# Performance work log

Measured on AMD Instinct MI355X. Metric: run time of the kernel, lower is better.

## Reference

```python
import jax, jax.numpy as jnp
import numpy as np
import math

N, E, C, NB, NEL, NG = 8192, 131072, 64, 8, 4, 16
R_MAX, AVG_NEI, P_CUT, NL, SH = 5.0, 16.0, 6, 2, 16


def _sph(u):
    # real spherical harmonics l=0..3, component normalization (sum_m Y_lm^2 = 2l+1 on unit sphere)
    x, y, z = u[:, 0], u[:, 1], u[:, 2]
    s3, s15, s5 = math.sqrt(3.0), math.sqrt(15.0), math.sqrt(5.0)
    s105, s7 = math.sqrt(105.0), math.sqrt(7.0)
    c35, c21 = math.sqrt(35.0 / 8.0), math.sqrt(21.0 / 8.0)
    Y = [jnp.ones_like(x),
         s3 * x, s3 * y, s3 * z,
         s15 * x * y, s15 * y * z, 0.5 * s5 * (3 * z * z - 1), s15 * x * z, 0.5 * s15 * (x * x - y * y),
         c35 * y * (3 * x * x - y * y), s105 * x * y * z, c21 * y * (5 * z * z - 1),
         0.5 * s7 * (5 * z ** 3 - 3 * z), c21 * x * (5 * z * z - 1),
         0.5 * s105 * z * (x * x - y * y), c35 * x * (x * x - 3 * y * y)]
    return jnp.stack(Y, axis=-1)  # [E,16]


def _bessel(r):
    k = jnp.arange(1, NB + 1, dtype=r.dtype)
    return math.sqrt(2.0 / R_MAX) * jnp.sin(k * jnp.pi * r[:, None] / R_MAX) / r[:, None]


def _poly_cutoff(r):
    p = float(P_CUT)
    x = r / R_MAX
    f = (1.0 - 0.5 * (p + 1) * (p + 2) * x ** p + p * (p + 2) * x ** (p + 1)
         - 0.5 * p * (p + 1) * x ** (p + 2))
    return f * (x < 1.0)


def setup_inputs() -> dict:
    key = jax.random.key(0)
    ks = jax.random.split(key, 16)
    sc = lambda fan: 1.0 / math.sqrt(fan)
    return {
        "pos": 2.0 * jax.random.normal(ks[0], (N, 3), jnp.float32),
        "atom_types": jax.random.randint(ks[1], (N,), 0, NEL),
        "edge_index": jax.random.randint(ks[2], (2, E), 0, N),
        "batch": jnp.sort(jax.random.randint(ks[3], (N,), 0, NG)),
        "W_embed": jax.random.normal(ks[4], (NEL, C), jnp.float32),
        "W_r1": sc(NB) * jax.random.normal(ks[5], (NL, NB, 64), jnp.float32),
        "W_r2": sc(64) * jax.random.normal(ks[6], (NL, 64, 64), jnp.float32),
        "W_r3": sc(64) * jax.random.normal(ks[7], (NL, 64, C), jnp.float32),
        "W_sc": sc(C) * jax.random.normal(ks[8], (NL, NEL, C, C), jnp.float32),
        "w_prod": 0.5 * jax.random.normal(ks[9], (NL, NEL, 4), jnp.float32),
        "w_ro0": sc(C) * jax.random.normal(ks[10], (C,), jnp.float32),
        "W_ro1a": sc(C) * jax.random.normal(ks[11], (C, 16), jnp.float32),
        "w_ro1b": sc(16) * jax.random.normal(ks[12], (16,), jnp.float32),
    }


def reference(pos, atom_types, edge_index, batch, W_embed, W_r1, W_r2, W_r3,
              W_sc, w_prod, w_ro0, W_ro1a, w_ro1b):
    src, dst = edge_index[0], edge_index[1]
    vec = pos[dst] - pos[src]                      # [E,3]
    r = jnp.sqrt(jnp.sum(vec * vec, -1) + 1e-12)   # [E]
    Y = _sph(vec / r[:, None])                     # [E,SH]
    edge_feats = _bessel(r) * _poly_cutoff(r)[:, None]  # [E,NB]
    h = W_embed[atom_types]                        # one-hot @ W == lookup, [N,C]
    energies = [jnp.zeros((NG,), pos.dtype)]       # pair_repulsion disabled
    for i in range(NL):
        Rw = jax.nn.silu(edge_feats @ W_r1[i])
        Rw = jax.nn.silu(Rw @ W_r2[i])
        Rw = Rw @ W_r3[i]                          # radial MLP weights [E,C]
        # gather-TP-scatter: message [E,C,SH] -> node A [N,C,SH]
        m = (Rw * h[src])[:, :, None] * Y[:, None, :]
        A = jax.ops.segment_sum(m.reshape(E, C * SH), dst,
                                num_segments=N).reshape(N, C, SH) / AVG_NEI
        sc_feat = jnp.einsum('nc,ncd->nd', h, W_sc[i][atom_types])  # element-dep skip
        inv = jnp.stack([A[:, :, 0],
                         jnp.sum(A[:, :, 1:4] ** 2, -1),
                         jnp.sum(A[:, :, 4:9] ** 2, -1),
                         jnp.sum(A[:, :, 9:16] ** 2, -1)], axis=-1)  # [N,C,4]
        h = jnp.einsum('ncj,nj->nc', inv, w_prod[i][atom_types]) + sc_feat
        if i < NL - 1:
            e_node = h @ w_ro0                     # linear readout
        else:
            e_node = jax.nn.silu(h @ W_ro1a) @ w_ro1b  # gated MLP readout
        energies.append(jax.ops.segment_sum(e_node, batch, num_segments=NG))
    contributions = jnp.stack(energies, -1)        # [NG, NL+1]
    return jnp.sum(contributions, -1)              # total energy per graph
```

## Files before the change

### kernel.cpp

```cpp
#include <hip/hip_runtime.h>
#include <hip/hip_bf16.h>
#include <math.h>

#define N_NODES 8192
#define N_EDGES 131072
#define NGRP 16
#define NLAY 2
#define NELM 4
constexpr float INV_AVG = 1.0f / 16.0f;
constexpr float PI_F = 3.14159265358979323846f;

#define CV_POS   0
#define CV_EMB   24576
#define CV_SC    42240
#define CV_PROD  75008
#define CV_RO0   75040
#define CV_RO1A  75104
#define CV_RO1B  76128
#define CVT_N    76144

#define SWZ_PER_L 10240
#define SWZ_N     20480

#define B_CVT  230
#define B_SWZ  80
#define B_HIST 512
#define CVT_WORK 58736

typedef __hip_bfloat16 bf16;
typedef __attribute__((ext_vector_type(8))) short bf16x8;
typedef __attribute__((ext_vector_type(4))) float f32x4;

__device__ __forceinline__ float silu_f(float x){ return x / (1.0f + __expf(-x)); }
__device__ __forceinline__ float bfbits2f(unsigned short u){
  return __uint_as_float(((unsigned)u) << 16);
}
__device__ __forceinline__ void unpack2(unsigned u, float& lo, float& hi){
  lo = __uint_as_float(u << 16);
  hi = __uint_as_float(u & 0xffff0000u);
}
__device__ __forceinline__ short f2bs(float v){
  union { bf16 b; short s; } u; u.b = __float2bfloat16(v); return u.s;
}
__device__ __forceinline__ float ldf(const void* p, int i, int flag){
  if (flag) return bfbits2f(((const unsigned short*)p)[i]);
  return ((const float*)p)[i];
}
__device__ __forceinline__ int detect_fl(const void* pos){
  int lane = threadIdx.x & 63;
  const unsigned short* u = (const unsigned short*)pos;
  float va = bfbits2f(u[2*lane]), vb = bfbits2f(u[2*lane+1]);
  bool bad = !(fabsf(va) <= 1000.0f) || !(fabsf(vb) <= 1000.0f);
  return (__ballot(bad) == 0ull) ? 1 : 0;
}
__device__ __forceinline__ void WSYNC(){ __builtin_amdgcn_wave_barrier(); }

__device__ __forceinline__ void gl_lds4(const void* g, void* l){
  __builtin_amdgcn_global_load_lds(
      (const __attribute__((address_space(1))) unsigned*)g,
      (__attribute__((address_space(3))) unsigned*)l, 4, 0, 0);
}

__global__ void k_setup1(const void* __restrict__ pos, const void* __restrict__ Wemb,
                         const void* __restrict__ Wsc, const void* __restrict__ wprod,
                         const void* __restrict__ wro0, const void* __restrict__ Wro1a,
                         const void* __restrict__ wro1b, const void* __restrict__ Wr1,
                         const void* __restrict__ Wr2, const void* __restrict__ Wr3,
                         const int* __restrict__ dstp, float* __restrict__ cv,
                         short* __restrict__ swz, int* __restrict__ deg){
  int b = blockIdx.x, tix = threadIdx.x;
  if (b >= B_CVT + B_SWZ){
    int e = (b - B_CVT - B_SWZ)*256 + tix;
    atomicAdd(&deg[dstp[e]], 1);
    return;
  }
  int fl = detect_fl(pos);
  if (b < B_CVT){
    int i = b*256 + tix;
    if (i < 24576){ cv[CV_POS + i] = ldf(pos, i, fl); return; }
    if (i < 24832){ int j=i-24576; cv[CV_EMB + j] = ldf(Wemb, j, fl); return; }
    if (i < 57600){ int j=i-24832; cv[CV_SC  + j] = ldf(Wsc,  j, fl); return; }
    if (i < 57632){ int j=i-57600; cv[CV_PROD+ j] = ldf(wprod,j, fl); return; }
    if (i < 57696){ int j=i-57632; cv[CV_RO0 + j] = ldf(wro0, j, fl); return; }
    if (i < 58720){ int j=i-57696; cv[CV_RO1A+ j] = ldf(Wro1a,j, fl); return; }
    if (i < CVT_WORK){ int j=i-58720; cv[CV_RO1B+ j] = ldf(wro1b,j, fl); return; }
    return;
  }
  int i = (b - B_CVT)*256 + tix;
  int l = i / SWZ_PER_L, w = i % SWZ_PER_L;
  float v;
  if (w < 2048){
    int t = w >> 9, q = (w >> 7) & 3, n = (w >> 3) & 15, j = w & 7;
    int k = q*8 + j;
    v = (k < 8) ? ldf(Wr1, l*512 + k*64 + t*16 + n, fl) : 0.0f;
  } else if (w < 6144){
    int w2 = w - 2048;
    int nt = w2 >> 10, kt = (w2 >> 9) & 1, q = (w2 >> 7) & 3, n = (w2 >> 3) & 15, j = w2 & 7;
    int k = kt*32 + q*8 + j;
    v = ldf(Wr2, l*4096 + k*64 + nt*16 + n, fl);
  } else {
    int w3 = w - 6144;
    int nt = w3 >> 10, kt = (w3 >> 9) & 1, q = (w3 >> 7) & 3, n = (w3 >> 3) & 15, j = w3 & 7;
    int k = kt*32 + q*8 + j;
    v = ldf(Wr3, l*4096 + k*64 + nt*16 + n, fl);
  }
  swz[i] = f2bs(v);
}

__global__ void k_scan(const int* __restrict__ deg, int* __restrict__ row_start,
                       int* __restrict__ cursor, float* __restrict__ ene){
  __shared__ int lds[1024];
  int t = threadIdx.x;
  if (t < NGRP) ene[t] = 0.0f;
  int v[8]; int tot = 0;
#pragma unroll
  for (int k = 0; k < 8; k++){ v[k] = deg[t*8+k]; tot += v[k]; }
  lds[t] = tot; __syncthreads();
  for (int off = 1; off < 1024; off <<= 1){
    int x = (t >= off) ? lds[t-off] : 0;
    __syncthreads();
    lds[t] += x;
    __syncthreads();
  }
  int base = lds[t] - tot;
#pragma unroll
  for (int k = 0; k < 8; k++){ row_start[t*8+k] = base; cursor[t*8+k] = base; base += v[k]; }
  if (t == 1023) row_start[N_NODES] = base;
}

__global__ void k_fillgeom(const int* __restrict__ ei, int* __restrict__ cursor,
                           const float* __restrict__ posf, const int* __restrict__ types,
                           int* __restrict__ sslot, unsigned char* __restrict__ tsl,
                           unsigned short* __restrict__ Yb, float* __restrict__ rbuf){
  int e = blockIdx.x*256 + threadIdx.x;
  int s = ei[e], d = ei[N_EDGES + e];
  int slot = atomicAdd(&cursor[d], 1);
  sslot[slot] = s;
  tsl[slot] = (unsigned char)types[s];
  float vx = posf[d*3+0] - posf[s*3+0];
  float vy = posf[d*3+1] - posf[s*3+1];
  float vz = posf[d*3+2] - posf[s*3+2];
  float r = sqrtf(vx*vx + vy*vy + vz*vz + 1e-12f);
  float ir = 1.0f / r;
  float x = vx*ir, y = vy*ir, z = vz*ir;
  const float s3 = 1.7320508075688772f, s15 = 3.872983346207417f, s5 = 2.23606797749979f;
  const float s105 = 10.246950765959598f, s7 = 2.6457513110645907f;
  const float c35 = 2.091650066335189f, c21 = 1.6201851746019651f;
  float x2 = x*x, y2 = y*y, z2 = z*z;
  float ys[16] = {
    1.0f, s3*x, s3*y, s3*z,
    s15*x*y, s15*y*z, 0.5f*s5*(3.0f*z2-1.0f), s15*x*z,
    0.5f*s15*(x2-y2), c35*y*(3.0f*x2-y2), s105*x*y*z, c21*y*(5.0f*z2-1.0f),
    0.5f*s7*(5.0f*z2*z-3.0f*z), c21*x*(5.0f*z2-1.0f), 0.5f*s105*z*(x2-y2),
    c35*x*(x2-3.0f*y2) };
  union { bf16 b[16]; uint4 u[2]; } pk;
#pragma unroll
  for (int k = 0; k < 16; k++) pk.b[k] = __float2bfloat16(ys[k]);
  uint4* yp = (uint4*)(Yb + (size_t)slot*16);
  yp[0] = pk.u[0];
  yp[1] = pk.u[1];
  rbuf[slot] = r;
}

#define ROWS 72
template<int LAYER_KIND>
__global__ void __launch_bounds__(256) k_gu(const short* __restrict__ sw,
        const float* __restrict__ rbuf, const unsigned char* __restrict__ tsl,
        const int* __restrict__ sslot, const float* __restrict__ h_old,
        float* __restrict__ h_new, const unsigned short* __restrict__ Yb,
        const int* __restrict__ row_start, const int* __restrict__ types,
        const float* __restrict__ Wsc, const float* __restrict__ wprod,
        const float* __restrict__ wemb, const float* __restrict__ wro0,
        const float* __restrict__ Wro1a, const float* __restrict__ wro1b,
        const int* __restrict__ batch, float* __restrict__ ene){
  __shared__ __align__(16) short A_[4][16*ROWS];
  __shared__ __align__(16) float hS[LAYER_KIND ? 4 : 1][16][64];
  __shared__ __align__(16) unsigned short yS[4][16][16];
  __shared__ float ebins[NGRP];
  __shared__ float hn_l[LAYER_KIND ? 4 : 1][64];
  int tix = threadIdx.x;
  if (tix < NGRP) ebins[tix] = 0.0f;
  __syncthreads();
  int wv = tix >> 6, lane = tix & 63;
  int q = lane >> 4, nn = lane & 15;
  int n = blockIdx.x * 4 + wv;
  int beg = row_start[n], end = row_start[n + 1];
  short* A = A_[wv];

  const bf16x8* S1 = (const bf16x8*)(sw);
  const bf16x8* S2 = (const bf16x8*)(sw + 2048);
  const bf16x8* S3 = (const bf16x8*)(sw + 6144);

  float e0=0.f, e1=0.f, e2=0.f, e3=0.f;
  if (LAYER_KIND == 0){
    e0 = wemb[lane]; e1 = wemb[64+lane]; e2 = wemb[128+lane]; e3 = wemb[192+lane];
  }

  float acc[16];
#pragma unroll
  for (int s = 0; s < 16; s++) acc[s] = 0.0f;

  for (int cb = beg; cb < end; cb += 16){
    int cnt = min(16, end - cb);
    WSYNC();
    const char* ysrc = (const char*)Yb + (size_t)cb*32 + lane*4;
    gl_lds4(ysrc,       &yS[wv][0][0]);
    gl_lds4(ysrc + 256, &yS[wv][8][0]);
    int tv = 0;
    if (LAYER_KIND == 0){
      tv = (int)tsl[min(cb + nn, N_EDGES - 1)];
    } else {
      int sv = sslot[min(cb + nn, N_EDGES - 1)];
      for (int i = 0; i < cnt; i++){
        int src = __builtin_amdgcn_readlane(sv, i);
        gl_lds4(h_old + (size_t)src*64 + lane, &hS[wv][i][0]);
      }
    }
    {
      float r = rbuf[min(cb + nn, N_EDGES - 1)];
      float xc = r * 0.2f;
      float f = 0.0f;
      if (xc < 1.0f){
        float x3 = xc*xc*xc, x6 = x3*x3, x7 = x6*xc, x8 = x7*xc;
        f = 1.0f - 28.0f*x6 + 48.0f*x7 - 21.0f*x8;
      }
      float bs = 0.6324555320336759f * f / r;
      float t0 = PI_F * r * 0.2f;
      bf16x8 af1 = {0,0,0,0,0,0,0,0};
      if (q == 0){
#pragma unroll
        for (int j = 0; j < 8; j++) af1[j] = f2bs(bs * __sinf((float)(j+1) * t0));
      }
      f32x4 macc[4];
#pragma unroll
      for (int t = 0; t < 4; t++){
        bf16x8 b = S1[t*64 + q*16 + nn];
        f32x4 z = {0.f,0.f,0.f,0.f};
        macc[t] = __builtin_amdgcn_mfma_f32_16x16x32_bf16(af1, b, z, 0, 0, 0);
      }
#pragma unroll
      for (int t = 0; t < 4; t++)
#pragma unroll
        for (int rg = 0; rg < 4; rg++)
          A[(q*4+rg)*ROWS + t*16 + nn] = f2bs(silu_f(macc[t][rg]));
      WSYNC();
      bf16x8 a0 = *(const bf16x8*)&A[nn*ROWS + 0*32 + q*8];
      bf16x8 a1 = *(const bf16x8*)&A[nn*ROWS + 1*32 + q*8];
      WSYNC();
#pragma unroll
      for (int t = 0; t < 4; t++){
        f32x4 z = {0.f,0.f,0.f,0.f};
        bf16x8 b0 = S2[t*128 + 0*64 + q*16 + nn];
        bf16x8 b1 = S2[t*128 + 1*64 + q*16 + nn];
        z = __builtin_amdgcn_mfma_f32_16x16x32_bf16(a0, b0, z, 0, 0, 0);
        z = __builtin_amdgcn_mfma_f32_16x16x32_bf16(a1, b1, z, 0, 0, 0);
        macc[t] = z;
      }
#pragma unroll
      for (int t = 0; t < 4; t++)
#pragma unroll
        for (int rg = 0; rg < 4; rg++)
          A[(q*4+rg)*ROWS + t*16 + nn] = f2bs(silu_f(macc[t][rg]));
      WSYNC();
      a0 = *(const bf16x8*)&A[nn*ROWS + 0*32 + q*8];
      a1 = *(const bf16x8*)&A[nn*ROWS + 1*32 + q*8];
      WSYNC();
#pragma unroll
      for (int t = 0; t < 4; t++){
        f32x4 z = {0.f,0.f,0.f,0.f};
        bf16x8 b0 = S3[t*128 + 0*64 + q*16 + nn];
        bf16x8 b1 = S3[t*128 + 1*64 + q*16 + nn];
        z = __builtin_amdgcn_mfma_f32_16x16x32_bf16(a0, b0, z, 0, 0, 0);
        z = __builtin_amdgcn_mfma_f32_16x16x32_bf16(a1, b1, z, 0, 0, 0);
        macc[t] = z;
      }
#pragma unroll
      for (int t = 0; t < 4; t++)
#pragma unroll
        for (int rg = 0; rg < 4; rg++)
          A[(q*4+rg)*ROWS + t*16 + nn] = f2bs(macc[t][rg]);
      WSYNC();
    }
    asm volatile("s_waitcnt vmcnt(0)" ::: "memory");
    __builtin_amdgcn_sched_barrier(0);
    for (int i = 0; i < cnt; i++){
      float rw = bfbits2f((unsigned short)A[i*ROWS + lane]);
      float hv;
      if (LAYER_KIND == 0){
        int ty = __builtin_amdgcn_readlane(tv, i);
        hv = (ty & 2) ? ((ty & 1) ? e3 : e2) : ((ty & 1) ? e1 : e0);
      } else {
        hv = hS[wv][i][lane];
      }
      float g = rw * hv;
      const uint4* yq = (const uint4*)&yS[wv][i][0];
      uint4 ya = yq[0], yb = yq[1];
      float lo, hi;
      unpack2(ya.x, lo, hi); acc[0]  += g*lo; acc[1]  += g*hi;
      unpack2(ya.y, lo, hi); acc[2]  += g*lo; acc[3]  += g*hi;
      unpack2(ya.z, lo, hi); acc[4]  += g*lo; acc[5]  += g*hi;
      unpack2(ya.w, lo, hi); acc[6]  += g*lo; acc[7]  += g*hi;
      unpack2(yb.x, lo, hi); acc[8]  += g*lo; acc[9]  += g*hi;
      unpack2(yb.y, lo, hi); acc[10] += g*lo; acc[11] += g*hi;
      unpack2(yb.z, lo, hi); acc[12] += g*lo; acc[13] += g*hi;
      unpack2(yb.w, lo, hi); acc[14] += g*lo; acc[15] += g*hi;
    }
  }
#pragma unroll
  for (int s = 0; s < 16; s++) acc[s] *= INV_AVG;

  int ty = __builtin_amdgcn_readfirstlane(types[n]);
  const float* Ws = Wsc + (size_t)ty*4096;
  const float* hrow = (LAYER_KIND == 0) ? (wemb + ty*64) : (h_old + (size_t)n*64);
  float sc0 = 0.f, sc1 = 0.f, sc2 = 0.f, sc3 = 0.f;
#pragma unroll
  for (int c = 0; c < 64; c += 4){
    sc0 += hrow[c+0] * Ws[(c+0)*64 + lane];
    sc1 += hrow[c+1] * Ws[(c+1)*64 + lane];
    sc2 += hrow[c+2] * Ws[(c+2)*64 + lane];
    sc3 += hrow[c+3] * Ws[(c+3)*64 + lane];
  }
  float sc = (sc0 + sc1) + (sc2 + sc3);

  float inv0 = acc[0];
  float inv1 = acc[1]*acc[1] + acc[2]*acc[2] + acc[3]*acc[3];
  float inv2 = acc[4]*acc[4] + acc[5]*acc[5] + acc[6]*acc[6] + acc[7]*acc[7]
             + acc[8]*acc[8];
  float inv3 = acc[9]*acc[9] + acc[10]*acc[10] + acc[11]*acc[11] + acc[12]*acc[12]
             + acc[13]*acc[13] + acc[14]*acc[14] + acc[15]*acc[15];
  const float* wp = wprod + ty*4;
  float hn = inv0*wp[0] + inv1*wp[1] + inv2*wp[2] + inv3*wp[3] + sc;
  if (LAYER_KIND == 0)
    h_new[(size_t)n*64 + lane] = hn;

  float ev;
  if (LAYER_KIND == 0){
    float p = hn * wro0[lane];
#pragma unroll
    for (int off = 32; off >= 1; off >>= 1) p += __shfl_xor(p, off, 64);
    ev = p;
  } else {
    hn_l[wv][lane] = hn;
    int j = lane & 15;
    float pj = 0.0f;
#pragma unroll
    for (int c = 0; c < 64; c++)
      pj += hn_l[wv][c] * Wro1a[c*16 + j];
    float evj = silu_f(pj) * wro1b[j];
    evj += __shfl_xor(evj, 8, 64);
    evj += __shfl_xor(evj, 4, 64);
    evj += __shfl_xor(evj, 2, 64);
    evj += __shfl_xor(evj, 1, 64);
    ev = evj;
  }
  if (lane == 0) atomicAdd(&ebins[batch[n]], ev);
  __syncthreads();
  if (tix < NGRP){
    float v = ebins[tix];
    if (v != 0.0f) atomicAdd(&ene[tix], v);
  }
}

__global__ void k_out(const float* __restrict__ ene, const void* __restrict__ pos,
                      void* __restrict__ out){
  int fl = detect_fl(pos);
  int t = threadIdx.x;
  if (t < NGRP){
    if (fl) ((bf16*)out)[t] = __float2bfloat16(ene[t]);
    else    ((float*)out)[t] = ene[t];
  }
}

static inline size_t rup(size_t x){ return (x + 255) & ~(size_t)255; }

extern "C" void kernel_launch(void* const* d_in, const int* in_sizes, int n_in,
                              void* d_out, int out_size, void* d_ws, size_t ws_size,
                              hipStream_t stream) {
  const void* pos   = d_in[0];
  const int*  types = (const int*)d_in[1];
  const int*  ei    = (const int*)d_in[2];
  const int*  batch = (const int*)d_in[3];
  const void* Wemb  = d_in[4];
  const void* Wr1   = d_in[5];
  const void* Wr2   = d_in[6];
  const void* Wr3   = d_in[7];
  const void* Wsc   = d_in[8];
  const void* wprod = d_in[9];
  const void* wro0  = d_in[10];
  const void* Wro1a = d_in[11];
  const void* wro1b = d_in[12];

  char* w = (char*)d_ws;
  float* cv       = (float*)w; w += rup((size_t)CVT_N*4);
  short* swz      = (short*)w; w += rup((size_t)SWZ_N*2);
  float* ene      = (float*)w; w += 256;
  int*   deg      = (int*)  w; w += rup((size_t)N_NODES*4);
  int*   row_start= (int*)  w; w += rup((size_t)(N_NODES+1)*4);
  int*   cursor   = (int*)  w; w += rup((size_t)N_NODES*4);
  int*   sslot    = (int*)  w; w += rup((size_t)N_EDGES*4);
  unsigned char* tsl = (unsigned char*)w; w += rup((size_t)N_EDGES);
  float* hbuf     = (float*)w; w += rup((size_t)N_NODES*64*4);
  float* rbuf     = (float*)w; w += rup((size_t)N_EDGES*4);
  unsigned short* Yb = (unsigned short*)w; w += rup((size_t)N_EDGES*16*2);
  w += 4096;

  hipMemsetAsync(deg, 0, N_NODES*4, stream);

  const int* dstp = ei + N_EDGES;
  k_setup1<<<B_CVT + B_SWZ + B_HIST, 256, 0, stream>>>(
      pos, Wemb, Wsc, wprod, wro0, Wro1a, wro1b, Wr1, Wr2, Wr3, dstp, cv, swz, deg);
  k_scan<<<1, 1024, 0, stream>>>(deg, row_start, cursor, ene);
  k_fillgeom<<<N_EDGES/256, 256, 0, stream>>>(ei, cursor, cv + CV_POS, types,
      sslot, tsl, Yb, rbuf);

  k_gu<0><<<N_NODES/4, 256, 0, stream>>>(swz, rbuf, tsl, sslot,
      hbuf , hbuf , Yb, row_start, types,
      cv + CV_SC, cv + CV_PROD, cv + CV_EMB,
      cv + CV_RO0, cv + CV_RO1A, cv + CV_RO1B, batch, ene);
  k_gu<1><<<N_NODES/4, 256, 0, stream>>>(swz + SWZ_PER_L, rbuf, tsl, sslot,
      hbuf , hbuf , Yb, row_start, types,
      cv + CV_SC + (size_t)NELM*4096, cv + CV_PROD + NELM*4, cv + CV_EMB,
      cv + CV_RO0, cv + CV_RO1A, cv + CV_RO1B, batch, ene);

  k_out<<<1, 64, 0, stream>>>(ene, pos, d_out);
}
```

Before: 200.7 us.

## Run one wave per node block and spread energy atomics over eight bins

The gather-update kernels now launch one 64-thread block per node instead of four waves per 256-thread block. The per-block LDS energy bins and the __syncthreads barriers go away. Each node's energy is atomically added into one of eight replicated global bin sets, chosen by node index, and k_out sums the eight sets at the end. The aim is to stop fast waves waiting on slow, high-degree nodes in the same block, and to spread atomic contention. The cost is more global atomics and more, smaller blocks, which may raise scheduling overhead.

After: 191.0 us. -4.8%, faster.

```diff
diff --git a/kernel.cpp b/kernel.cpp
--- a/kernel.cpp
+++ b/kernel.cpp
@@ -108,10 +108,10 @@
 }
 
 __global__ void k_scan(const int* __restrict__ deg, int* __restrict__ row_start,
-                       int* __restrict__ cursor, float* __restrict__ ene){
+                       int* __restrict__ cursor, float* __restrict__ ene2){
   __shared__ int lds[1024];
   int t = threadIdx.x;
-  if (t < NGRP) ene[t] = 0.0f;
+  if (t < 8*NGRP) ene2[t] = 0.0f;
   int v[8]; int tot = 0;
 #pragma unroll
   for (int k = 0; k < 8; k++){ v[k] = deg[t*8+k]; tot += v[k]; }
@@ -164,7 +164,7 @@
 
 #define ROWS 72
 template<int LAYER_KIND>
-__global__ void __launch_bounds__(256) k_gu(const short* __restrict__ sw,
+__global__ void __launch_bounds__(64, 4) k_gu(const short* __restrict__ sw,
         const float* __restrict__ rbuf, const unsigned char* __restrict__ tsl,
         const int* __restrict__ sslot, const float* __restrict__ h_old,
         float* __restrict__ h_new, const unsigned short* __restrict__ Yb,
@@ -172,20 +172,16 @@
         const float* __restrict__ Wsc, const float* __restrict__ wprod,
         const float* __restrict__ wemb, const float* __restrict__ wro0,
         const float* __restrict__ Wro1a, const float* __restrict__ wro1b,
-        const int* __restrict__ batch, float* __restrict__ ene){
-  __shared__ __align__(16) short A_[4][16*ROWS];
-  __shared__ __align__(16) float hS[LAYER_KIND ? 4 : 1][16][64];
-  __shared__ __align__(16) unsigned short yS[4][16][16];
-  __shared__ float ebins[NGRP];
-  __shared__ float hn_l[LAYER_KIND ? 4 : 1][64];
-  int tix = threadIdx.x;
-  if (tix < NGRP) ebins[tix] = 0.0f;
-  __syncthreads();
-  int wv = tix >> 6, lane = tix & 63;
+        const int* __restrict__ batch, float* __restrict__ ene2){
+  __shared__ __align__(16) short A_[16*ROWS];
+  __shared__ __align__(16) float hS[LAYER_KIND ? 16 : 1][64];
+  __shared__ __align__(16) unsigned short yS[16][16];
+  __shared__ float hn_l[64];
+  int lane = threadIdx.x;
   int q = lane >> 4, nn = lane & 15;
-  int n = blockIdx.x * 4 + wv;
+  int n = blockIdx.x;
   int beg = row_start[n], end = row_start[n + 1];
-  short* A = A_[wv];
+  short* A = A_;
 
   const bf16x8* S1 = (const bf16x8*)(sw);
   const bf16x8* S2 = (const bf16x8*)(sw + 2048);
@@ -204,8 +200,8 @@
     int cnt = min(16, end - cb);
     WSYNC();
     const char* ysrc = (const char*)Yb + (size_t)cb*32 + lane*4;
-    gl_lds4(ysrc,       &yS[wv][0][0]);
-    gl_lds4(ysrc + 256, &yS[wv][8][0]);
+    gl_lds4(ysrc,       &yS[0][0]);
+    gl_lds4(ysrc + 256, &yS[8][0]);
     int tv = 0;
     if (LAYER_KIND == 0){
       tv = (int)tsl[min(cb + nn, N_EDGES - 1)];
@@ -213,7 +209,7 @@
       int sv = sslot[min(cb + nn, N_EDGES - 1)];
       for (int i = 0; i < cnt; i++){
         int src = __builtin_amdgcn_readlane(sv, i);
-        gl_lds4(h_old + (size_t)src*64 + lane, &hS[wv][i][0]);
+        gl_lds4(h_old + (size_t)src*64 + lane, &hS[i][0]);
       }
     }
     {
@@ -290,10 +286,10 @@
         int ty = __builtin_amdgcn_readlane(tv, i);
         hv = (ty & 2) ? ((ty & 1) ? e3 : e2) : ((ty & 1) ? e1 : e0);
       } else {
-        hv = hS[wv][i][lane];
+        hv = hS[i][lane];
       }
       float g = rw * hv;
-      const uint4* yq = (const uint4*)&yS[wv][i][0];
+      const uint4* yq = (const uint4*)&yS[i][0];
       uint4 ya = yq[0], yb = yq[1];
       float lo, hi;
       unpack2(ya.x, lo, hi); acc[0]  += g*lo; acc[1]  += g*hi;
@@ -340,12 +336,13 @@
     for (int off = 32; off >= 1; off >>= 1) p += __shfl_xor(p, off, 64);
     ev = p;
   } else {
-    hn_l[wv][lane] = hn;
+    hn_l[lane] = hn;
+    WSYNC();
     int j = lane & 15;
     float pj = 0.0f;
 #pragma unroll
     for (int c = 0; c < 64; c++)
-      pj += hn_l[wv][c] * Wro1a[c*16 + j];
+      pj += hn_l[c] * Wro1a[c*16 + j];
     float evj = silu_f(pj) * wro1b[j];
     evj += __shfl_xor(evj, 8, 64);
     evj += __shfl_xor(evj, 4, 64);
@@ -353,21 +350,19 @@
     evj += __shfl_xor(evj, 1, 64);
     ev = evj;
   }
-  if (lane == 0) atomicAdd(&ebins[batch[n]], ev);
-  __syncthreads();
-  if (tix < NGRP){
-    float v = ebins[tix];
-    if (v != 0.0f) atomicAdd(&ene[tix], v);
-  }
-}
-
-__global__ void k_out(const float* __restrict__ ene, const void* __restrict__ pos,
+  if (lane == 0) atomicAdd(&ene2[(n & 7)*NGRP + batch[n]], ev);
+}
+
+__global__ void k_out(const float* __restrict__ ene2, const void* __restrict__ pos,
                       void* __restrict__ out){
   int fl = detect_fl(pos);
   int t = threadIdx.x;
   if (t < NGRP){
-    if (fl) ((bf16*)out)[t] = __float2bfloat16(ene[t]);
-    else    ((float*)out)[t] = ene[t];
+    float v = 0.0f;
+#pragma unroll
+    for (int k = 0; k < 8; k++) v += ene2[k*NGRP + t];
+    if (fl) ((bf16*)out)[t] = __float2bfloat16(v);
+    else    ((float*)out)[t] = v;
   }
 }
 
@@ -393,7 +388,7 @@
   char* w = (char*)d_ws;
   float* cv       = (float*)w; w += rup((size_t)CVT_N*4);
   short* swz      = (short*)w; w += rup((size_t)SWZ_N*2);
-  float* ene      = (float*)w; w += 256;
+  float* ene2     = (float*)w; w += 512;
   int*   deg      = (int*)  w; w += rup((size_t)N_NODES*4);
   int*   row_start= (int*)  w; w += rup((size_t)(N_NODES+1)*4);
   int*   cursor   = (int*)  w; w += rup((size_t)N_NODES*4);
@@ -409,18 +404,18 @@
   const int* dstp = ei + N_EDGES;
   k_setup1<<<B_CVT + B_SWZ + B_HIST, 256, 0, stream>>>(
       pos, Wemb, Wsc, wprod, wro0, Wro1a, wro1b, Wr1, Wr2, Wr3, dstp, cv, swz, deg);
-  k_scan<<<1, 1024, 0, stream>>>(deg, row_start, cursor, ene);
+  k_scan<<<1, 1024, 0, stream>>>(deg, row_start, cursor, ene2);
   k_fillgeom<<<N_EDGES/256, 256, 0, stream>>>(ei, cursor, cv + CV_POS, types,
       sslot, tsl, Yb, rbuf);
 
-  k_gu<0><<<N_NODES/4, 256, 0, stream>>>(swz, rbuf, tsl, sslot,
+  k_gu<0><<<N_NODES, 64, 0, stream>>>(swz, rbuf, tsl, sslot,
       hbuf , hbuf , Yb, row_start, types,
       cv + CV_SC, cv + CV_PROD, cv + CV_EMB,
-      cv + CV_RO0, cv + CV_RO1A, cv + CV_RO1B, batch, ene);
-  k_gu<1><<<N_NODES/4, 256, 0, stream>>>(swz + SWZ_PER_L, rbuf, tsl, sslot,
+      cv + CV_RO0, cv + CV_RO1A, cv + CV_RO1B, batch, ene2);
+  k_gu<1><<<N_NODES, 64, 0, stream>>>(swz + SWZ_PER_L, rbuf, tsl, sslot,
       hbuf , hbuf , Yb, row_start, types,
       cv + CV_SC + (size_t)NELM*4096, cv + CV_PROD + NELM*4, cv + CV_EMB,
-      cv + CV_RO0, cv + CV_RO1A, cv + CV_RO1B, batch, ene);
-
-  k_out<<<1, 64, 0, stream>>>(ene, pos, d_out);
-}
+      cv + CV_RO0, cv + CV_RO1A, cv + CV_RO1B, batch, ene2);
+
+  k_out<<<1, 64, 0, stream>>>(ene2, pos, d_out);
+}
```
